# Kernel optimization log

Hardware: AMD Instinct MI355X
Metric: run time of the kernel (lower is better)

Reference implementation:

```python
import jax, jax.numpy as jnp
import numpy as np

PAD = 0.1
RESO = 128           # plane_resolution
HID = 128            # hidden_dim
CDIM = 128           # c_dim
NBLK = 5             # n_blocks
PLANES = (('xz', (0, 2)), ('xy', (0, 1)), ('yz', (1, 2)))


def normalize_coordinate(p, dims):
    # p: (B,T,3) -> (B,T,2) in [0, 1)
    xy = p[..., list(dims)] / (1.0 + PAD + 1e-3) + 0.5
    return jnp.clip(xy, 0.0, 1.0 - 1e-5)


def coordinate2index(xy, reso):
    g = (xy * reso).astype(jnp.int32)          # (B,T,2)
    return g[..., 0] + reso * g[..., 1]        # (B,T) flat cell index


def scatter_max_gather(vals, idx, n_cells):
    # vals: (B,T,F), idx: (B,T) -> per-cell max gathered back to points (B,T,F)
    B, T, F = vals.shape
    flat_idx = (idx + jnp.arange(B, dtype=idx.dtype)[:, None] * n_cells).reshape(-1)
    fea = jax.ops.segment_max(vals.reshape(B * T, F), flat_idx, num_segments=B * n_cells)
    return fea[flat_idx].reshape(B, T, F)


def scatter_mean_plane(c, idx, n_cells):
    # c: (B,T,C), idx: (B,T) -> (B, n_cells, C); empty cells stay 0
    B, T, C = c.shape
    flat_idx = (idx + jnp.arange(B, dtype=idx.dtype)[:, None] * n_cells).reshape(-1)
    s = jax.ops.segment_sum(c.reshape(B * T, C), flat_idx, num_segments=B * n_cells)
    cnt = jax.ops.segment_sum(jnp.ones((B * T,), c.dtype), flat_idx, num_segments=B * n_cells)
    return (s / jnp.maximum(cnt, 1.0)[:, None]).reshape(B, n_cells, C)


def resnet_block(x, W0, b0, W1, b1, Ws):
    # ResnetBlockFC(2H -> H), size_h = H, shortcut = Linear(no bias)
    net = jax.nn.relu(x) @ W0 + b0
    dx = jax.nn.relu(net) @ W1 + b1
    return x @ Ws + dx


def setup_inputs() -> dict:
    key = jax.random.key(0)
    ks = jax.random.split(key, 10)
    B, T = 2, 32768
    s = 0.05
    return {
        'p': jax.random.uniform(ks[0], (B, T, 3), jnp.float32, -0.5, 0.5),
        'fc_pos_W': s * jax.random.normal(ks[1], (3, 2 * HID), jnp.float32),
        'fc_pos_b': s * jax.random.normal(ks[2], (2 * HID,), jnp.float32),
        'blocks_W0': s * jax.random.normal(ks[3], (NBLK, 2 * HID, HID), jnp.float32),
        'blocks_b0': s * jax.random.normal(ks[4], (NBLK, HID), jnp.float32),
        'blocks_W1': s * jax.random.normal(ks[5], (NBLK, HID, HID), jnp.float32),
        'blocks_b1': s * jax.random.normal(ks[6], (NBLK, HID), jnp.float32),
        'blocks_Ws': s * jax.random.normal(ks[7], (NBLK, 2 * HID, HID), jnp.float32),
        'fc_c_W': s * jax.random.normal(ks[8], (HID, CDIM), jnp.float32),
        'fc_c_b': s * jax.random.normal(ks[9], (CDIM,), jnp.float32),
    }


def reference(p, fc_pos_W, fc_pos_b, blocks_W0, blocks_b0, blocks_W1, blocks_b1,
              blocks_Ws, fc_c_W, fc_c_b):
    B, T, _ = p.shape
    R2 = RESO * RESO
    index = {k: coordinate2index(normalize_coordinate(p, d), RESO) for k, d in PLANES}

    net = p @ fc_pos_W + fc_pos_b                       # (B,T,2H)
    net = resnet_block(net, blocks_W0[0], blocks_b0[0],
                       blocks_W1[0], blocks_b1[0], blocks_Ws[0])  # (B,T,H)
    for i in range(1, NBLK):
        pooled = sum(scatter_max_gather(net, index[k], R2) for k, _ in PLANES)
        net = jnp.concatenate([net, pooled], axis=-1)   # (B,T,2H)
        net = resnet_block(net, blocks_W0[i], blocks_b0[i],
                           blocks_W1[i], blocks_b1[i], blocks_Ws[i])

    c = net @ fc_c_W + fc_c_b                           # (B,T,C)
    planes = []
    for k, _ in PLANES:  # order: xz, xy, yz
        fea = scatter_mean_plane(c, index[k], R2)       # (B,R2,C)
        planes.append(fea.transpose(0, 2, 1).reshape(B, CDIM, RESO, RESO))
    return jnp.stack(planes)                            # (3,B,C,R,R)
```

## Files before the change

kernel.cpp:

```cpp
#include <hip/hip_runtime.h>

#define TT 65536
#define R2 16384

typedef _Float16 f16x8 __attribute__((ext_vector_type(8)));
typedef float    f32x4 __attribute__((ext_vector_type(4)));
typedef unsigned u32x4 __attribute__((ext_vector_type(4)));

#define MFMA16 __builtin_amdgcn_mfma_f32_16x16x32_f16

#define LTS 136
#define LTW 2176

__device__ __forceinline__ unsigned short f2h(float f){
    _Float16 h = (_Float16)f;
    return __builtin_bit_cast(unsigned short, h);
}
__device__ __forceinline__ float h2f(unsigned short u){
    return (float)__builtin_bit_cast(_Float16, u);
}
__device__ __forceinline__ unsigned relu2(unsigned w){
    unsigned s = w & 0x80008000u;
    unsigned mask = ((s >> 15) * 0x7FFFu) | s;
    return w & ~mask;
}
__device__ __forceinline__ float nrm(float a){
    float v = a / 1.101f + 0.5f;
    v = fmaxf(v, 0.0f);
    v = fminf(v, 0.99999f);
    return v;
}
#define VMCNT0() asm volatile("s_waitcnt vmcnt(0)" ::: "memory")
#define LGKM0()  asm volatile("s_waitcnt lgkmcnt(0)" ::: "memory")
#define SB0()    __builtin_amdgcn_sched_barrier(0)

__global__ __launch_bounds__(256) void k_repack(const float* __restrict__ W0,
        const float* __restrict__ W1, const float* __restrict__ Ws,
        const float* __restrict__ Wc, unsigned short* __restrict__ out,
        int* __restrict__ cnt){
    __shared__ unsigned short lh[4096];
    int b = blockIdx.x, tid = threadIdx.x;

    int gid = b*256 + tid;
    if (gid < 24576){ u32x4 z = {0,0,0,0}; ((u32x4*)cnt)[gid] = z; }

    const float* src; int obase;
    if (b < 100){
        int i = b/20, rr = b%20;
        if (rr < 8){       src = W0 + (size_t)i*32768 + rr*4096;      obase = i*81920 + rr*4096; }
        else if (rr < 12){ int ks=rr-8;  src = W1 + (size_t)i*16384 + ks*4096; obase = i*81920 + 32768 + ks*4096; }
        else {             int ks=rr-12; src = Ws + (size_t)i*32768 + ks*4096; obase = i*81920 + 49152 + ks*4096; }
    } else { int ks = b-100; src = Wc + ks*4096; obase = 409600 + ks*4096; }

    #pragma unroll
    for (int m = 0; m < 16; m++){
        int gi = m*256 + tid;
        lh[gi] = f2h(src[gi]);
    }
    __syncthreads();

    #pragma unroll
    for (int g2 = 0; g2 < 2; g2++){
        int base = tid*16 + g2*8;
        int l = (base >> 3) & 63, t = (base >> 9) & 7;
        int n = t*16 + (l & 15), kb = (l >> 4)*8;
        unsigned short h[8];
        #pragma unroll
        for (int j = 0; j < 8; j++) h[j] = lh[(kb + j)*128 + n];
        u32x4 pk;
        #pragma unroll
        for (int q = 0; q < 4; q++)
            pk[q] = (unsigned)h[2*q] | ((unsigned)h[2*q+1] << 16);
        *(u32x4*)(&out[obase + base]) = pk;
    }
}

__global__ __launch_bounds__(256) void k_idxhist(const float* __restrict__ p,
        int* __restrict__ idx, int* __restrict__ cnt){
    int pt = blockIdx.x*256 + threadIdx.x;
    float p0 = p[pt*3+0], p1 = p[pt*3+1], p2 = p[pt*3+2];
    int g0 = (int)(nrm(p0)*128.f);
    int g1 = (int)(nrm(p1)*128.f);
    int g2 = (int)(nrm(p2)*128.f);
    int i0 = g0 + 128*g2, i1 = g0 + 128*g1, i2 = g1 + 128*g2;
    idx[0*TT + pt] = i0;
    idx[1*TT + pt] = i1;
    idx[2*TT + pt] = i2;
    int b14 = (pt >> 15) << 14;
    atomicAdd(&cnt[0*32768 + b14 + i0], 1);
    atomicAdd(&cnt[1*32768 + b14 + i1], 1);
    atomicAdd(&cnt[2*32768 + b14 + i2], 1);
}

__global__ __launch_bounds__(1024) void k_scan(const int* cnt,
        int* __restrict__ cs, int* cp){
    __shared__ int wsum[16];
    int pl = blockIdx.x, tid = threadIdx.x;
    int lane = tid & 63, wid = tid >> 6;
    const int* c = cnt + pl*32768;
    int v[32], tot = 0;
    #pragma unroll
    for (int j = 0; j < 32; j++){ v[j] = c[tid*32 + j]; tot += v[j]; }
    int x = tot;
    #pragma unroll
    for (int off = 1; off < 64; off <<= 1){
        int y = __shfl_up(x, off, 64);
        if (lane >= off) x += y;
    }
    if (lane == 63) wsum[wid] = x;
    __syncthreads();
    int woff = 0;
    #pragma unroll
    for (int j = 0; j < 16; j++) woff += (j < wid) ? wsum[j] : 0;
    int run = woff + x - tot;
    #pragma unroll
    for (int j = 0; j < 32; j++){
        cs[pl*32769 + tid*32 + j] = run;
        cp[pl*32768 + tid*32 + j] = run;
        run += v[j];
    }
    if (tid == 1023) cs[pl*32769 + 32768] = TT;
}

__global__ __launch_bounds__(256) void k_scatter(const int* __restrict__ idx,
        int* __restrict__ cp, int* __restrict__ srt){
    int pt = blockIdx.x*256 + threadIdx.x;
    int b14 = (pt >> 15) << 14;
    #pragma unroll
    for (int pl = 0; pl < 3; pl++){
        int pos = atomicAdd(&cp[pl*32768 + b14 + idx[pl*TT + pt]], 1);
        srt[pl*TT + pos] = pt;
    }
}

__global__ __launch_bounds__(256) void k_pool3(const unsigned short* __restrict__ xb,
        const int* __restrict__ srt, const int* __restrict__ cs,
        unsigned short* __restrict__ mxp){
    int pl = blockIdx.y;
    const int* srtp = srt + (size_t)pl*TT;
    const int* csp  = cs  + (size_t)pl*32769;
    int lane = threadIdx.x & 63, w = threadIdx.x >> 6;
    int g = lane >> 4, l16 = lane & 15;
    int cbase = (blockIdx.x*4 + w)*4;
    for (int c = cbase; c < cbase + 4; c++){
        int s = csp[c], e = csp[c+1];
        if (s == e) continue;
        f16x8 m;
        #pragma unroll
        for (int j = 0; j < 8; j++) m[j] = (_Float16)(-65504.f);
        for (int i = s + g; i < e; i += 4){
            int pt = srtp[i];
            f16x8 v = *(const f16x8*)(xb + (size_t)pt*128 + l16*8);
            #pragma unroll
            for (int j = 0; j < 8; j++)
                m[j] = (v[j] > m[j]) ? v[j] : m[j];
        }
        #pragma unroll
        for (int sh = 16; sh <= 32; sh += 16){
            u32x4 um = __builtin_bit_cast(u32x4, m);
            u32x4 o;
            #pragma unroll
            for (int q = 0; q < 4; q++) o[q] = __shfl_xor(um[q], sh, 64);
            f16x8 vm = __builtin_bit_cast(f16x8, o);
            #pragma unroll
            for (int j = 0; j < 8; j++)
                m[j] = (vm[j] > m[j]) ? vm[j] : m[j];
        }
        if (g == 0)
            ((u32x4*)(mxp + ((size_t)pl*32768 + c)*128))[l16] =
                __builtin_bit_cast(u32x4, m);
    }
}

template<int MODE, int NW>
__device__ __forceinline__ void resnet_body(
        const unsigned short* __restrict__ xin,
        unsigned short* __restrict__ xout,
        const unsigned short* __restrict__ wp,
        const float* __restrict__ b0, const float* __restrict__ b1,
        const int* __restrict__ idx, const unsigned short* __restrict__ mxp,
        const float* __restrict__ pin, const float* __restrict__ fW,
        const float* __restrict__ fb,
        const unsigned short* __restrict__ wc, const float* __restrict__ bc,
        unsigned short* lw, unsigned short* lt){
    int tid = threadIdx.x, w = tid >> 6, lane = tid & 63;
    int quad = lane >> 4, l15 = lane & 15;
    int m0 = blockIdx.x*(NW*16) + w*16;
    unsigned short* ltw = lt + w*LTW;

    auto stage = [&](const unsigned short* src){
        #pragma unroll
        for (int i = 0; i < 32/NW; i++){
            int chunk = i*NW + w;
            __builtin_amdgcn_global_load_lds(
                (const __attribute__((address_space(1))) unsigned*)(src + chunk*512 + lane*8),
                (__attribute__((address_space(3))) unsigned*)(lw + chunk*512),
                16, 0, 0);
        }
    };
    auto gemm = [&](const f16x8* a, f32x4 (&ac)[8]){
        #pragma unroll
        for (int ks = 0; ks < 4; ks++){
            #pragma unroll
            for (int t = 0; t < 8; t++){
                f16x8 b = *(const f16x8*)&lw[((ks*8 + t)*64 + lane)*8];
                ac[t] = MFMA16(a[ks], b, ac[t], 0, 0, 0);
            }
        }
    };

    stage(wp);
    SB0();

    u32x4 xf[4]; f16x8 pf[4];
    u32x4 g0[4], g1[4], g2[4];
    if (MODE == 0){
        int row = m0 + l15;
        float p0 = pin[row*3+0], p1 = pin[row*3+1], p2 = pin[row*3+2];
        #pragma unroll
        for (int ks = 0; ks < 4; ks++){
            int c0 = ks*32 + quad*8;
            unsigned short hx[8], hp[8];
            #pragma unroll
            for (int h = 0; h < 2; h++){
                f32x4 w0 = *(const f32x4*)(fW + c0 + h*4);
                f32x4 w1 = *(const f32x4*)(fW + 256 + c0 + h*4);
                f32x4 w2 = *(const f32x4*)(fW + 512 + c0 + h*4);
                f32x4 bb = *(const f32x4*)(fb + c0 + h*4);
                f32x4 v0 = *(const f32x4*)(fW + 128 + c0 + h*4);
                f32x4 v1 = *(const f32x4*)(fW + 384 + c0 + h*4);
                f32x4 v2 = *(const f32x4*)(fW + 640 + c0 + h*4);
                f32x4 bp = *(const f32x4*)(fb + 128 + c0 + h*4);
                #pragma unroll
                for (int j = 0; j < 4; j++){
                    hx[h*4+j] = f2h(bb[j] + p0*w0[j] + p1*w1[j] + p2*w2[j]);
                    hp[h*4+j] = f2h(bp[j] + p0*v0[j] + p1*v1[j] + p2*v2[j]);
                }
            }
            unsigned short* dx = (unsigned short*)&xf[ks];
            unsigned short* dp = (unsigned short*)&pf[ks];
            #pragma unroll
            for (int j = 0; j < 8; j++){ dx[j] = hx[j]; dp[j] = hp[j]; }
        }
    } else {
        int row = m0 + l15;
        size_t rb = (size_t)row*128;
        #pragma unroll
        for (int ks = 0; ks < 4; ks++)
            xf[ks] = *(const u32x4*)(xin + rb + ks*32 + quad*8);
        int b14 = (row >> 15) << 14;
        const unsigned short* q0 = mxp + ((size_t)(0*32768 + b14 + idx[row]))*128;
        const unsigned short* q1 = mxp + ((size_t)(1*32768 + b14 + idx[TT + row]))*128;
        const unsigned short* q2 = mxp + ((size_t)(2*32768 + b14 + idx[2*TT + row]))*128;
        #pragma unroll
        for (int ks = 0; ks < 4; ks++){
            int col = ks*32 + quad*8;
            g0[ks] = *(const u32x4*)(q0 + col);
            g1[ks] = *(const u32x4*)(q1 + col);
            g2[ks] = *(const u32x4*)(q2 + col);
        }
    }

    f32x4 acc[8];
    #pragma unroll
    for (int t = 0; t < 8; t++){ f32x4 z = {0.f,0.f,0.f,0.f}; acc[t] = z; }

    if (MODE == 0){
        VMCNT0();
    } else {
        SB0();
        asm volatile("s_waitcnt vmcnt(16)" ::: "memory");
        SB0();
    }
    __syncthreads();

    {
        f16x8 a[4];
        #pragma unroll
        for (int ks = 0; ks < 4; ks++){
            u32x4 u = xf[ks];
            u.x = relu2(u.x); u.y = relu2(u.y); u.z = relu2(u.z); u.w = relu2(u.w);
            a[ks] = __builtin_bit_cast(f16x8, u);
        }
        gemm(a, acc);
    }
    if (MODE != 0){
        #pragma unroll
        for (int ks = 0; ks < 4; ks++){
            f16x8 a = __builtin_bit_cast(f16x8, g0[ks]);
            f16x8 b = __builtin_bit_cast(f16x8, g1[ks]);
            f16x8 c = __builtin_bit_cast(f16x8, g2[ks]);
            pf[ks] = a + b + c;
        }
    }
    __syncthreads();
    stage(wp + 16384);
    VMCNT0(); __syncthreads();

    {
        f16x8 a[4];
        #pragma unroll
        for (int ks = 0; ks < 4; ks++){
            u32x4 u = __builtin_bit_cast(u32x4, pf[ks]);
            u.x = relu2(u.x); u.y = relu2(u.y); u.z = relu2(u.z); u.w = relu2(u.w);
            a[ks] = __builtin_bit_cast(f16x8, u);
        }
        gemm(a, acc);
    }
    __syncthreads();
    stage(wp + 32768);
    VMCNT0(); __syncthreads();

    {
        float b0v[8];
        #pragma unroll
        for (int t = 0; t < 8; t++) b0v[t] = b0[t*16 + l15];
        #pragma unroll
        for (int t = 0; t < 8; t++)
            #pragma unroll
            for (int r = 0; r < 4; r++){
                float v = fmaxf(acc[t][r] + b0v[t], 0.f);
                ltw[(quad*4 + r)*LTS + t*16 + l15] = f2h(v);
            }
    }
    LGKM0();
    f32x4 acc2[8];
    {
        #pragma unroll
        for (int t = 0; t < 8; t++){
            float bv = b1[t*16 + l15];
            f32x4 iv = {bv, bv, bv, bv};
            acc2[t] = iv;
        }
    }
    #pragma unroll
    for (int ks = 0; ks < 4; ks++){
        f16x8 a0 = *(const f16x8*)&ltw[l15*LTS + ks*32 + quad*8];
        #pragma unroll
        for (int t = 0; t < 8; t++){
            f16x8 b = *(const f16x8*)&lw[((ks*8 + t)*64 + lane)*8];
            acc2[t] = MFMA16(a0, b, acc2[t], 0, 0, 0);
        }
    }
    __syncthreads();
    stage(wp + 49152);
    VMCNT0(); __syncthreads();

    {
        f16x8 a[4];
        #pragma unroll
        for (int ks = 0; ks < 4; ks++)
            a[ks] = __builtin_bit_cast(f16x8, xf[ks]);
        gemm(a, acc2);
    }
    __syncthreads();
    stage(wp + 65536);
    VMCNT0(); __syncthreads();

    gemm(pf, acc2);

    if (MODE != 2){
        #pragma unroll
        for (int t = 0; t < 8; t++)
            #pragma unroll
            for (int r = 0; r < 4; r++){
                int row = m0 + quad*4 + r;
                xout[(size_t)row*128 + t*16 + l15] = f2h(acc2[t][r]);
            }
        return;
    }
    __syncthreads();
    stage(wc);
    VMCNT0(); __syncthreads();

    #pragma unroll
    for (int t = 0; t < 8; t++)
        #pragma unroll
        for (int r = 0; r < 4; r++)
            ltw[(quad*4 + r)*LTS + t*16 + l15] = f2h(acc2[t][r]);
    LGKM0();
    f32x4 acc3[8];
    #pragma unroll
    for (int t = 0; t < 8; t++){
        float bv = bc[t*16 + l15];
        f32x4 iv = {bv, bv, bv, bv};
        acc3[t] = iv;
    }
    #pragma unroll
    for (int ks = 0; ks < 4; ks++){
        f16x8 a0 = *(const f16x8*)&ltw[l15*LTS + ks*32 + quad*8];
        #pragma unroll
        for (int t = 0; t < 8; t++){
            f16x8 b = *(const f16x8*)&lw[((ks*8 + t)*64 + lane)*8];
            acc3[t] = MFMA16(a0, b, acc3[t], 0, 0, 0);
        }
    }
    #pragma unroll
    for (int t = 0; t < 8; t++)
        #pragma unroll
        for (int r = 0; r < 4; r++){
            int row = m0 + quad*4 + r;
            xout[(size_t)row*128 + t*16 + l15] = f2h(acc3[t][r]);
        }
}

__global__ __launch_bounds__(256, 2) void k_resnet_head(
        unsigned short* __restrict__ xout, const unsigned short* __restrict__ wp,
        const float* __restrict__ b0, const float* __restrict__ b1,
        const float* __restrict__ pin, const float* __restrict__ fW,
        const float* __restrict__ fb){
    __shared__ __align__(16) unsigned short lw[16384];
    __shared__ __align__(16) unsigned short lt[8704];
    resnet_body<0,4>(nullptr, xout, wp, b0, b1, nullptr, nullptr,
                   pin, fW, fb, nullptr, nullptr, lw, lt);
}
__global__ __launch_bounds__(512, 2) void k_resnet_mid(
        const unsigned short* __restrict__ xin, unsigned short* __restrict__ xout,
        const unsigned short* __restrict__ wp,
        const float* __restrict__ b0, const float* __restrict__ b1,
        const int* __restrict__ idx, const unsigned short* __restrict__ mxp){
    __shared__ __align__(16) unsigned short lw[16384];
    __shared__ __align__(16) unsigned short lt[17408];
    resnet_body<1,8>(xin, xout, wp, b0, b1, idx, mxp,
                   nullptr, nullptr, nullptr, nullptr, nullptr, lw, lt);
}
__global__ __launch_bounds__(512, 2) void k_resnet_tail(
        const unsigned short* __restrict__ xin, unsigned short* __restrict__ xout,
        const unsigned short* __restrict__ wp,
        const float* __restrict__ b0, const float* __restrict__ b1,
        const int* __restrict__ idx, const unsigned short* __restrict__ mxp,
        const unsigned short* __restrict__ wc, const float* __restrict__ bc){
    __shared__ __align__(16) unsigned short lw[16384];
    __shared__ __align__(16) unsigned short lt[17408];
    resnet_body<2,8>(xin, xout, wp, b0, b1, idx, mxp,
                   nullptr, nullptr, nullptr, wc, bc, lw, lt);
}

__global__ __launch_bounds__(256) void k_psum3(const unsigned short* __restrict__ cb,
        const int* __restrict__ srt, const int* __restrict__ cs,
        float* __restrict__ out){
    __shared__ float ls[32*129];
    int pl = blockIdx.y;
    const int* srtp = srt + (size_t)pl*TT;
    const int* csp  = cs  + (size_t)pl*32769;
    int tid = threadIdx.x;
    int lane = tid & 63, w = tid >> 6;
    int g = lane >> 4, l16 = lane & 15;
    int c0 = blockIdx.x * 32;
    for (int cc = w*8; cc < w*8 + 8; cc++){
        int c = c0 + cc;
        int s = csp[c], e = csp[c+1];
        float fs[8];
        #pragma unroll
        for (int j = 0; j < 8; j++) fs[j] = 0.f;
        for (int i = s + g; i < e; i += 4){
            int pt = srtp[i];
            u32x4 v = *(const u32x4*)(cb + (size_t)pt*128 + l16*8);
            #pragma unroll
            for (int q = 0; q < 4; q++){
                unsigned u = v[q];
                fs[2*q]   += h2f((unsigned short)(u & 0xFFFF));
                fs[2*q+1] += h2f((unsigned short)(u >> 16));
            }
        }
        #pragma unroll
        for (int j = 0; j < 8; j++){
            fs[j] += __shfl_xor(fs[j], 16, 64);
            fs[j] += __shfl_xor(fs[j], 32, 64);
        }
        float rc = (e > s) ? 1.f/(float)(e - s) : 0.f;
        if (g == 0){
            #pragma unroll
            for (int j = 0; j < 8; j++) ls[cc*129 + l16*8 + j] = fs[j]*rc;
        }
    }
    __syncthreads();
    int pb = pl*2 + (c0 >> 14);
    float* o = out + (size_t)pb*128*R2 + (c0 & 16383);
    #pragma unroll
    for (int k = 0; k < 16; k++){
        int lin = k*256 + tid;
        int f = lin >> 5, cc = lin & 31;
        o[(size_t)f*R2 + cc] = ls[cc*129 + f];
    }
}

extern "C" void kernel_launch(void* const* d_in, const int* in_sizes, int n_in,
                              void* d_out, int out_size, void* d_ws, size_t ws_size,
                              hipStream_t stream) {
    const float* p        = (const float*)d_in[0];
    const float* fc_pos_W = (const float*)d_in[1];
    const float* fc_pos_b = (const float*)d_in[2];
    const float* bW0      = (const float*)d_in[3];
    const float* bb0      = (const float*)d_in[4];
    const float* bW1      = (const float*)d_in[5];
    const float* bb1      = (const float*)d_in[6];
    const float* bWs      = (const float*)d_in[7];
    const float* fc_c_W   = (const float*)d_in[8];
    const float* fc_c_b   = (const float*)d_in[9];
    float* out = (float*)d_out;

    char* ws = (char*)d_ws;
    int*            idx   = (int*)ws;
    unsigned short* net0  = (unsigned short*)(ws + 786432);
    unsigned short* net1  = (unsigned short*)(ws + 17563648);
    unsigned short* cbuf  = (unsigned short*)(ws + 34340864);
    int*            srt   = (int*)(ws + 51118080);
    int*            cs    = (int*)(ws + 51904512);
    int*            cp    = (int*)(ws + 52297744);
    unsigned short* wpack = (unsigned short*)(ws + 52690960);
    unsigned short* mxp   = (unsigned short*)(ws + 53542928);

    k_repack <<<104, 256, 0, stream>>>(bW0, bW1, bWs, fc_c_W, wpack, cp);
    k_idxhist<<<256, 256, 0, stream>>>(p, idx, cp);
    k_scan   <<<3, 1024, 0, stream>>>(cp, cs, cp);
    k_scatter<<<256, 256, 0, stream>>>(idx, cp, srt);

    k_resnet_head<<<1024, 256, 0, stream>>>(net0, wpack, bb0, bb1,
            p, fc_pos_W, fc_pos_b);

    k_pool3<<<dim3(2048, 3), 256, 0, stream>>>(net0, srt, cs, mxp);
    k_resnet_mid<<<512, 512, 0, stream>>>(net0, net1, wpack + 81920,
            bb0 + 128, bb1 + 128, idx, mxp);
    k_pool3<<<dim3(2048, 3), 256, 0, stream>>>(net1, srt, cs, mxp);
    k_resnet_mid<<<512, 512, 0, stream>>>(net1, net0, wpack + 163840,
            bb0 + 256, bb1 + 256, idx, mxp);
    k_pool3<<<dim3(2048, 3), 256, 0, stream>>>(net0, srt, cs, mxp);
    k_resnet_mid<<<512, 512, 0, stream>>>(net0, net1, wpack + 245760,
            bb0 + 384, bb1 + 384, idx, mxp);
    k_pool3<<<dim3(2048, 3), 256, 0, stream>>>(net1, srt, cs, mxp);
    k_resnet_tail<<<512, 512, 0, stream>>>(net1, cbuf, wpack + 327680,
            bb0 + 512, bb1 + 512, idx, mxp, wpack + 409600, fc_c_b);

    k_psum3<<<dim3(1024, 3), 256, 0, stream>>>(cbuf, srt, cs, out);
}
```

Before: 362.1 us.

## Scatter pooled maxima per point and write tail output in sorted order

k_pool3 now writes each cell's max back to every member point in a per-point pooled buffer, so the resnet mid kernels read pooled features contiguously instead of gathering through idx into the per-cell max table. The tail kernel writes its output three times, once per plane, at each point's sorted rank (recorded by k_scatter). This lets k_psum3 read sorted rows directly without the srt indirection. The cost is much more global write traffic (three full copies of the pooled and output features) and a larger workspace, all to get coalesced reads.

Result: slower. 383.6 us (+5.9%).

```diff
diff --git a/kernel.cpp b/kernel.cpp
--- a/kernel.cpp
+++ b/kernel.cpp
@@ -123,19 +123,20 @@
 }
 
 __global__ __launch_bounds__(256) void k_scatter(const int* __restrict__ idx,
-        int* __restrict__ cp, int* __restrict__ srt){
+        int* __restrict__ cp, int* __restrict__ srt, int* __restrict__ rnk){
     int pt = blockIdx.x*256 + threadIdx.x;
     int b14 = (pt >> 15) << 14;
     #pragma unroll
     for (int pl = 0; pl < 3; pl++){
         int pos = atomicAdd(&cp[pl*32768 + b14 + idx[pl*TT + pt]], 1);
         srt[pl*TT + pos] = pt;
+        rnk[pl*TT + pt] = pos;
     }
 }
 
 __global__ __launch_bounds__(256) void k_pool3(const unsigned short* __restrict__ xb,
         const int* __restrict__ srt, const int* __restrict__ cs,
-        unsigned short* __restrict__ mxp){
+        unsigned short* __restrict__ pp){
     int pl = blockIdx.y;
     const int* srtp = srt + (size_t)pl*TT;
     const int* csp  = cs  + (size_t)pl*32769;
@@ -166,9 +167,11 @@
             for (int j = 0; j < 8; j++)
                 m[j] = (vm[j] > m[j]) ? vm[j] : m[j];
         }
-        if (g == 0)
-            ((u32x4*)(mxp + ((size_t)pl*32768 + c)*128))[l16] =
-                __builtin_bit_cast(u32x4, m);
+        u32x4 pk = __builtin_bit_cast(u32x4, m);
+        for (int i = s + g; i < e; i += 4){
+            int pt = srtp[i];
+            ((u32x4*)(pp + ((size_t)pl*TT + pt)*128))[l16] = pk;
+        }
     }
 }
 
@@ -178,10 +181,11 @@
         unsigned short* __restrict__ xout,
         const unsigned short* __restrict__ wp,
         const float* __restrict__ b0, const float* __restrict__ b1,
-        const int* __restrict__ idx, const unsigned short* __restrict__ mxp,
+        const unsigned short* __restrict__ pp,
         const float* __restrict__ pin, const float* __restrict__ fW,
         const float* __restrict__ fb,
         const unsigned short* __restrict__ wc, const float* __restrict__ bc,
+        const int* __restrict__ rnk,
         unsigned short* lw, unsigned short* lt){
     int tid = threadIdx.x, w = tid >> 6, lane = tid & 63;
     int quad = lane >> 4, l15 = lane & 15;
@@ -248,16 +252,12 @@
         #pragma unroll
         for (int ks = 0; ks < 4; ks++)
             xf[ks] = *(const u32x4*)(xin + rb + ks*32 + quad*8);
-        int b14 = (row >> 15) << 14;
-        const unsigned short* q0 = mxp + ((size_t)(0*32768 + b14 + idx[row]))*128;
-        const unsigned short* q1 = mxp + ((size_t)(1*32768 + b14 + idx[TT + row]))*128;
-        const unsigned short* q2 = mxp + ((size_t)(2*32768 + b14 + idx[2*TT + row]))*128;
         #pragma unroll
         for (int ks = 0; ks < 4; ks++){
-            int col = ks*32 + quad*8;
-            g0[ks] = *(const u32x4*)(q0 + col);
-            g1[ks] = *(const u32x4*)(q1 + col);
-            g2[ks] = *(const u32x4*)(q2 + col);
+            int off = ks*32 + quad*8;
+            g0[ks] = *(const u32x4*)(pp + 0*(size_t)TT*128 + rb + off);
+            g1[ks] = *(const u32x4*)(pp + 1*(size_t)TT*128 + rb + off);
+            g2[ks] = *(const u32x4*)(pp + 2*(size_t)TT*128 + rb + off);
         }
     }
 
@@ -396,12 +396,17 @@
         }
     }
     #pragma unroll
-    for (int t = 0; t < 8; t++)
-        #pragma unroll
-        for (int r = 0; r < 4; r++){
-            int row = m0 + quad*4 + r;
-            xout[(size_t)row*128 + t*16 + l15] = f2h(acc3[t][r]);
-        }
+    for (int r = 0; r < 4; r++){
+        int row = m0 + quad*4 + r;
+        int p0 = rnk[0*TT + row], p1 = rnk[1*TT + row], p2 = rnk[2*TT + row];
+        #pragma unroll
+        for (int t = 0; t < 8; t++){
+            unsigned short v = f2h(acc3[t][r]);
+            xout[(0*(size_t)TT + p0)*128 + t*16 + l15] = v;
+            xout[(1*(size_t)TT + p1)*128 + t*16 + l15] = v;
+            xout[(2*(size_t)TT + p2)*128 + t*16 + l15] = v;
+        }
+    }
 }
 
 __global__ __launch_bounds__(256, 2) void k_resnet_head(
@@ -411,42 +416,42 @@
         const float* __restrict__ fb){
     __shared__ __align__(16) unsigned short lw[16384];
     __shared__ __align__(16) unsigned short lt[8704];
-    resnet_body<0,4>(nullptr, xout, wp, b0, b1, nullptr, nullptr,
-                   pin, fW, fb, nullptr, nullptr, lw, lt);
+    resnet_body<0,4>(nullptr, xout, wp, b0, b1, nullptr,
+                   pin, fW, fb, nullptr, nullptr, nullptr, lw, lt);
 }
 __global__ __launch_bounds__(512, 2) void k_resnet_mid(
         const unsigned short* __restrict__ xin, unsigned short* __restrict__ xout,
         const unsigned short* __restrict__ wp,
         const float* __restrict__ b0, const float* __restrict__ b1,
-        const int* __restrict__ idx, const unsigned short* __restrict__ mxp){
+        const unsigned short* __restrict__ pp){
     __shared__ __align__(16) unsigned short lw[16384];
     __shared__ __align__(16) unsigned short lt[17408];
-    resnet_body<1,8>(xin, xout, wp, b0, b1, idx, mxp,
-                   nullptr, nullptr, nullptr, nullptr, nullptr, lw, lt);
+    resnet_body<1,8>(xin, xout, wp, b0, b1, pp,
+                   nullptr, nullptr, nullptr, nullptr, nullptr, nullptr, lw, lt);
 }
 __global__ __launch_bounds__(512, 2) void k_resnet_tail(
         const unsigned short* __restrict__ xin, unsigned short* __restrict__ xout,
         const unsigned short* __restrict__ wp,
         const float* __restrict__ b0, const float* __restrict__ b1,
-        const int* __restrict__ idx, const unsigned short* __restrict__ mxp,
-        const unsigned short* __restrict__ wc, const float* __restrict__ bc){
+        const unsigned short* __restrict__ pp,
+        const unsigned short* __restrict__ wc, const float* __restrict__ bc,
+        const int* __restrict__ rnk){
     __shared__ __align__(16) unsigned short lw[16384];
     __shared__ __align__(16) unsigned short lt[17408];
-    resnet_body<2,8>(xin, xout, wp, b0, b1, idx, mxp,
-                   nullptr, nullptr, nullptr, wc, bc, lw, lt);
+    resnet_body<2,8>(xin, xout, wp, b0, b1, pp,
+                   nullptr, nullptr, nullptr, wc, bc, rnk, lw, lt);
 }
 
 __global__ __launch_bounds__(256) void k_psum3(const unsigned short* __restrict__ cb,
-        const int* __restrict__ srt, const int* __restrict__ cs,
-        float* __restrict__ out){
+        const int* __restrict__ cs, float* __restrict__ out){
     __shared__ float ls[32*129];
     int pl = blockIdx.y;
-    const int* srtp = srt + (size_t)pl*TT;
-    const int* csp  = cs  + (size_t)pl*32769;
+    const int* csp = cs + (size_t)pl*32769;
     int tid = threadIdx.x;
     int lane = tid & 63, w = tid >> 6;
     int g = lane >> 4, l16 = lane & 15;
     int c0 = blockIdx.x * 32;
+    const unsigned short* cbp = cb + (size_t)pl*TT*128;
     for (int cc = w*8; cc < w*8 + 8; cc++){
         int c = c0 + cc;
         int s = csp[c], e = csp[c+1];
@@ -454,8 +459,7 @@
         #pragma unroll
         for (int j = 0; j < 8; j++) fs[j] = 0.f;
         for (int i = s + g; i < e; i += 4){
-            int pt = srtp[i];
-            u32x4 v = *(const u32x4*)(cb + (size_t)pt*128 + l16*8);
+            u32x4 v = *(const u32x4*)(cbp + (size_t)i*128 + l16*8);
             #pragma unroll
             for (int q = 0; q < 4; q++){
                 unsigned u = v[q];
@@ -504,33 +508,34 @@
     int*            idx   = (int*)ws;
     unsigned short* net0  = (unsigned short*)(ws + 786432);
     unsigned short* net1  = (unsigned short*)(ws + 17563648);
-    unsigned short* cbuf  = (unsigned short*)(ws + 34340864);
-    int*            srt   = (int*)(ws + 51118080);
-    int*            cs    = (int*)(ws + 51904512);
-    int*            cp    = (int*)(ws + 52297744);
-    unsigned short* wpack = (unsigned short*)(ws + 52690960);
-    unsigned short* mxp   = (unsigned short*)(ws + 53542928);
+    unsigned short* cb3   = (unsigned short*)(ws + 34340864);
+    int*            srt   = (int*)(ws + 84672512);
+    int*            rnk   = (int*)(ws + 85458944);
+    int*            cs    = (int*)(ws + 86245376);
+    int*            cp    = (int*)(ws + 86638608);
+    unsigned short* wpack = (unsigned short*)(ws + 87031824);
+    unsigned short* ppool = (unsigned short*)(ws + 87883792);
 
     k_repack <<<104, 256, 0, stream>>>(bW0, bW1, bWs, fc_c_W, wpack, cp);
     k_idxhist<<<256, 256, 0, stream>>>(p, idx, cp);
     k_scan   <<<3, 1024, 0, stream>>>(cp, cs, cp);
-    k_scatter<<<256, 256, 0, stream>>>(idx, cp, srt);
+    k_scatter<<<256, 256, 0, stream>>>(idx, cp, srt, rnk);
 
     k_resnet_head<<<1024, 256, 0, stream>>>(net0, wpack, bb0, bb1,
             p, fc_pos_W, fc_pos_b);
 
-    k_pool3<<<dim3(2048, 3), 256, 0, stream>>>(net0, srt, cs, mxp);
+    k_pool3<<<dim3(2048, 3), 256, 0, stream>>>(net0, srt, cs, ppool);
     k_resnet_mid<<<512, 512, 0, stream>>>(net0, net1, wpack + 81920,
-            bb0 + 128, bb1 + 128, idx, mxp);
-    k_pool3<<<dim3(2048, 3), 256, 0, stream>>>(net1, srt, cs, mxp);
+            bb0 + 128, bb1 + 128, ppool);
+    k_pool3<<<dim3(2048, 3), 256, 0, stream>>>(net1, srt, cs, ppool);
     k_resnet_mid<<<512, 512, 0, stream>>>(net1, net0, wpack + 163840,
-            bb0 + 256, bb1 + 256, idx, mxp);
-    k_pool3<<<dim3(2048, 3), 256, 0, stream>>>(net0, srt, cs, mxp);
+            bb0 + 256, bb1 + 256, ppool);
+    k_pool3<<<dim3(2048, 3), 256, 0, stream>>>(net0, srt, cs, ppool);
     k_resnet_mid<<<512, 512, 0, stream>>>(net0, net1, wpack + 245760,
-            bb0 + 384, bb1 + 384, idx, mxp);
-    k_pool3<<<dim3(2048, 3), 256, 0, stream>>>(net1, srt, cs, mxp);
-    k_resnet_tail<<<512, 512, 0, stream>>>(net1, cbuf, wpack + 327680,
-            bb0 + 512, bb1 + 512, idx, mxp, wpack + 409600, fc_c_b);
-
-    k_psum3<<<dim3(1024, 3), 256, 0, stream>>>(cbuf, srt, cs, out);
-}
+            bb0 + 384, bb1 + 384, ppool);
+    k_pool3<<<dim3(2048, 3), 256, 0, stream>>>(net1, srt, cs, ppool);
+    k_resnet_tail<<<512, 512, 0, stream>>>(net1, cb3, wpack + 327680,
+            bb0 + 512, bb1 + 512, ppool, wpack + 409600, fc_c_b, rnk);
+
+    k_psum3<<<dim3(1024, 3), 256, 0, stream>>>(cb3, cs, out);
+}
```

## Double-buffer weight staging in LDS halves to overlap loads with MFMA

Applied to the files above, without the earlier changes.

Splits the 32KB LDS weight buffer into two 16KB halves and streams each weight matrix in half-sized chunks, so the next half is loaded via global_load_lds while MFMAs run on the other half. The full vmcnt(0) plus syncthreads waits become partial vmcnt waits and raw barriers. Bias loads are hoisted to the kernel start. This adds more barriers and relies on exact vmcnt counting, which could hide hazards if the counts are wrong.

New measurement: 379.1 us. +4.7%, slower.

```diff
diff --git a/kernel.cpp b/kernel.cpp
--- a/kernel.cpp
+++ b/kernel.cpp
@@ -187,29 +187,61 @@
     int quad = lane >> 4, l15 = lane & 15;
     int m0 = blockIdx.x*(NW*16) + w*16;
     unsigned short* ltw = lt + w*LTW;
-
-    auto stage = [&](const unsigned short* src){
-        #pragma unroll
-        for (int i = 0; i < 32/NW; i++){
-            int chunk = i*NW + w;
+    unsigned short* s0 = lw;
+    unsigned short* s1 = lw + 8192;
+
+    auto stage_half = [&](const unsigned short* srch, unsigned short* dsth){
+        #pragma unroll
+        for (int i = 0; i < 16/NW; i++){
+            int c = i*NW + w;
             __builtin_amdgcn_global_load_lds(
-                (const __attribute__((address_space(1))) unsigned*)(src + chunk*512 + lane*8),
-                (__attribute__((address_space(3))) unsigned*)(lw + chunk*512),
+                (const __attribute__((address_space(1))) unsigned*)(srch + c*512 + lane*8),
+                (__attribute__((address_space(3))) unsigned*)(dsth + c*512),
                 16, 0, 0);
         }
     };
-    auto gemm = [&](const f16x8* a, f32x4 (&ac)[8]){
-        #pragma unroll
-        for (int ks = 0; ks < 4; ks++){
-            #pragma unroll
-            for (int t = 0; t < 8; t++){
-                f16x8 b = *(const f16x8*)&lw[((ks*8 + t)*64 + lane)*8];
-                ac[t] = MFMA16(a[ks], b, ac[t], 0, 0, 0);
-            }
+    auto gemm_half = [&](f16x8 a0, f16x8 a1, const unsigned short* lws,
+                         f32x4 (&ac)[8]){
+        #pragma unroll
+        for (int t = 0; t < 8; t++){
+            f16x8 b = *(const f16x8*)&lws[((t)*64 + lane)*8];
+            ac[t] = MFMA16(a0, b, ac[t], 0, 0, 0);
+        }
+        #pragma unroll
+        for (int t = 0; t < 8; t++){
+            f16x8 b = *(const f16x8*)&lws[((8 + t)*64 + lane)*8];
+            ac[t] = MFMA16(a1, b, ac[t], 0, 0, 0);
         }
     };
-
-    stage(wp);
+    auto ringwaitHL = [&](){
+        SB0();
+        if constexpr (NW == 8) asm volatile("s_waitcnt vmcnt(2)" ::: "memory");
+        else                   asm volatile("s_waitcnt vmcnt(4)" ::: "memory");
+        __builtin_amdgcn_s_barrier();
+        SB0();
+    };
+    auto ringwait0 = [&](){
+        SB0();
+        asm volatile("s_waitcnt vmcnt(0)" ::: "memory");
+        __builtin_amdgcn_s_barrier();
+        SB0();
+    };
+    auto postbar = [&](){ SB0(); __builtin_amdgcn_s_barrier(); SB0(); };
+    auto reluc = [&](u32x4 u){
+        u.x = relu2(u.x); u.y = relu2(u.y); u.z = relu2(u.z); u.w = relu2(u.w);
+        return __builtin_bit_cast(f16x8, u);
+    };
+
+    float b0v[8], b1v[8], bcv[8];
+    #pragma unroll
+    for (int t = 0; t < 8; t++){ b0v[t] = b0[t*16 + l15]; b1v[t] = b1[t*16 + l15]; }
+    if (MODE == 2){
+        #pragma unroll
+        for (int t = 0; t < 8; t++) bcv[t] = bc[t*16 + l15];
+    }
+
+    stage_half(wp,        s0);
+    stage_half(wp + 8192, s1);
     SB0();
 
     u32x4 xf[4]; f16x8 pf[4];
@@ -266,24 +298,16 @@
     for (int t = 0; t < 8; t++){ f32x4 z = {0.f,0.f,0.f,0.f}; acc[t] = z; }
 
     if (MODE == 0){
-        VMCNT0();
+        SB0(); VMCNT0();
+        __builtin_amdgcn_s_barrier(); SB0();
     } else {
         SB0();
         asm volatile("s_waitcnt vmcnt(16)" ::: "memory");
-        SB0();
-    }
-    __syncthreads();
-
-    {
-        f16x8 a[4];
-        #pragma unroll
-        for (int ks = 0; ks < 4; ks++){
-            u32x4 u = xf[ks];
-            u.x = relu2(u.x); u.y = relu2(u.y); u.z = relu2(u.z); u.w = relu2(u.w);
-            a[ks] = __builtin_bit_cast(f16x8, u);
-        }
-        gemm(a, acc);
-    }
+        __builtin_amdgcn_s_barrier(); SB0();
+    }
+
+    gemm_half(reluc(xf[0]), reluc(xf[1]), s0, acc);
+    gemm_half(reluc(xf[2]), reluc(xf[3]), s1, acc);
     if (MODE != 0){
         #pragma unroll
         for (int ks = 0; ks < 4; ks++){
@@ -293,71 +317,70 @@
             pf[ks] = a + b + c;
         }
     }
-    __syncthreads();
-    stage(wp + 16384);
-    VMCNT0(); __syncthreads();
-
+    postbar();
+
+    stage_half(wp + 16384,        s0);
+    stage_half(wp + 16384 + 8192, s1);
+    ringwaitHL();
     {
-        f16x8 a[4];
-        #pragma unroll
-        for (int ks = 0; ks < 4; ks++){
-            u32x4 u = __builtin_bit_cast(u32x4, pf[ks]);
-            u.x = relu2(u.x); u.y = relu2(u.y); u.z = relu2(u.z); u.w = relu2(u.w);
-            a[ks] = __builtin_bit_cast(f16x8, u);
-        }
-        gemm(a, acc);
-    }
-    __syncthreads();
-    stage(wp + 32768);
-    VMCNT0(); __syncthreads();
-
+        u32x4 u0 = __builtin_bit_cast(u32x4, pf[0]);
+        u32x4 u1 = __builtin_bit_cast(u32x4, pf[1]);
+        gemm_half(reluc(u0), reluc(u1), s0, acc);
+    }
+    postbar();
+    stage_half(wp + 32768, s0);
+    ringwaitHL();
     {
-        float b0v[8];
-        #pragma unroll
-        for (int t = 0; t < 8; t++) b0v[t] = b0[t*16 + l15];
-        #pragma unroll
-        for (int t = 0; t < 8; t++)
-            #pragma unroll
-            for (int r = 0; r < 4; r++){
-                float v = fmaxf(acc[t][r] + b0v[t], 0.f);
-                ltw[(quad*4 + r)*LTS + t*16 + l15] = f2h(v);
-            }
-    }
+        u32x4 u2 = __builtin_bit_cast(u32x4, pf[2]);
+        u32x4 u3 = __builtin_bit_cast(u32x4, pf[3]);
+        gemm_half(reluc(u2), reluc(u3), s1, acc);
+    }
+    postbar();
+    stage_half(wp + 32768 + 8192, s1);
+    #pragma unroll
+    for (int t = 0; t < 8; t++)
+        #pragma unroll
+        for (int r = 0; r < 4; r++){
+            float v = fmaxf(acc[t][r] + b0v[t], 0.f);
+            ltw[(quad*4 + r)*LTS + t*16 + l15] = f2h(v);
+        }
+    f32x4 acc2[8];
+    #pragma unroll
+    for (int t = 0; t < 8; t++){ f32x4 iv = {b1v[t],b1v[t],b1v[t],b1v[t]}; acc2[t] = iv; }
     LGKM0();
-    f32x4 acc2[8];
+    ringwaitHL();
     {
-        #pragma unroll
-        for (int t = 0; t < 8; t++){
-            float bv = b1[t*16 + l15];
-            f32x4 iv = {bv, bv, bv, bv};
-            acc2[t] = iv;
-        }
-    }
-    #pragma unroll
-    for (int ks = 0; ks < 4; ks++){
-        f16x8 a0 = *(const f16x8*)&ltw[l15*LTS + ks*32 + quad*8];
-        #pragma unroll
-        for (int t = 0; t < 8; t++){
-            f16x8 b = *(const f16x8*)&lw[((ks*8 + t)*64 + lane)*8];
-            acc2[t] = MFMA16(a0, b, acc2[t], 0, 0, 0);
-        }
-    }
-    __syncthreads();
-    stage(wp + 49152);
-    VMCNT0(); __syncthreads();
-
+        f16x8 a0 = *(const f16x8*)&ltw[l15*LTS + 0*32 + quad*8];
+        f16x8 a1 = *(const f16x8*)&ltw[l15*LTS + 1*32 + quad*8];
+        gemm_half(a0, a1, s0, acc2);
+    }
+    postbar();
+    stage_half(wp + 49152, s0);
+    ringwaitHL();
     {
-        f16x8 a[4];
-        #pragma unroll
-        for (int ks = 0; ks < 4; ks++)
-            a[ks] = __builtin_bit_cast(f16x8, xf[ks]);
-        gemm(a, acc2);
-    }
-    __syncthreads();
-    stage(wp + 65536);
-    VMCNT0(); __syncthreads();
-
-    gemm(pf, acc2);
+        f16x8 a2 = *(const f16x8*)&ltw[l15*LTS + 2*32 + quad*8];
+        f16x8 a3 = *(const f16x8*)&ltw[l15*LTS + 3*32 + quad*8];
+        gemm_half(a2, a3, s1, acc2);
+    }
+    postbar();
+    stage_half(wp + 49152 + 8192, s1);
+    ringwaitHL();
+    gemm_half(__builtin_bit_cast(f16x8, xf[0]),
+              __builtin_bit_cast(f16x8, xf[1]), s0, acc2);
+    postbar();
+    stage_half(wp + 65536, s0);
+    ringwaitHL();
+    gemm_half(__builtin_bit_cast(f16x8, xf[2]),
+              __builtin_bit_cast(f16x8, xf[3]), s1, acc2);
+    postbar();
+    stage_half(wp + 65536 + 8192, s1);
+    ringwaitHL();
+    gemm_half(pf[0], pf[1], s0, acc2);
+    postbar();
+    if (MODE == 2) stage_half(wc, s0);
+    if (MODE == 2) ringwaitHL();
+    else           ringwait0();
+    gemm_half(pf[2], pf[3], s1, acc2);
 
     if (MODE != 2){
         #pragma unroll
@@ -369,31 +392,29 @@
             }
         return;
     }
-    __syncthreads();
-    stage(wc);
-    VMCNT0(); __syncthreads();
-
+
+    postbar();
+    stage_half(wc + 8192, s1);
     #pragma unroll
     for (int t = 0; t < 8; t++)
         #pragma unroll
         for (int r = 0; r < 4; r++)
             ltw[(quad*4 + r)*LTS + t*16 + l15] = f2h(acc2[t][r]);
+    f32x4 acc3[8];
+    #pragma unroll
+    for (int t = 0; t < 8; t++){ f32x4 iv = {bcv[t],bcv[t],bcv[t],bcv[t]}; acc3[t] = iv; }
     LGKM0();
-    f32x4 acc3[8];
-    #pragma unroll
-    for (int t = 0; t < 8; t++){
-        float bv = bc[t*16 + l15];
-        f32x4 iv = {bv, bv, bv, bv};
-        acc3[t] = iv;
-    }
-    #pragma unroll
-    for (int ks = 0; ks < 4; ks++){
-        f16x8 a0 = *(const f16x8*)&ltw[l15*LTS + ks*32 + quad*8];
-        #pragma unroll
-        for (int t = 0; t < 8; t++){
-            f16x8 b = *(const f16x8*)&lw[((ks*8 + t)*64 + lane)*8];
-            acc3[t] = MFMA16(a0, b, acc3[t], 0, 0, 0);
-        }
+    ringwaitHL();
+    {
+        f16x8 a0 = *(const f16x8*)&ltw[l15*LTS + 0*32 + quad*8];
+        f16x8 a1 = *(const f16x8*)&ltw[l15*LTS + 1*32 + quad*8];
+        gemm_half(a0, a1, s0, acc3);
+    }
+    ringwait0();
+    {
+        f16x8 a2 = *(const f16x8*)&ltw[l15*LTS + 2*32 + quad*8];
+        f16x8 a3 = *(const f16x8*)&ltw[l15*LTS + 3*32 + quad*8];
+        gemm_half(a2, a3, s1, acc3);
     }
     #pragma unroll
     for (int t = 0; t < 8; t++)
```
